# Kernel optimization log

Hardware: AMD Instinct MI355X
Metric: run time of the kernel (lower is better)

The kernel has to match this reference:

```python
import jax, jax.numpy as jnp
import numpy as np
import math

B, H, S, D = 2, 16, 2048, 128
INV_SCALE = math.sqrt(D)  # divisor applied to QK^T logits (dropout_p = 0.0)


def setup_inputs() -> dict:
    key = jax.random.key(0)
    kq, kk, kv = jax.random.split(key, 3)
    return {
        "query": jax.random.normal(kq, (B, H, S, D), dtype=jnp.float32),
        "key": jax.random.normal(kk, (B, H, S, D), dtype=jnp.float32),
        "value": jax.random.normal(kv, (B, H, S, D), dtype=jnp.float32),
    }


def reference(query, key, value):
    # v1 = Q @ K^T ; v2 = v1 / inv_scale ; v3 = softmax(v2, -1) ; dropout(p=0) is identity ; out = v3 @ V
    scores = jnp.einsum("bhqd,bhkd->bhqk", query, key) / INV_SCALE  # [B,H,Sq,Sk]
    probs = jax.nn.softmax(scores, axis=-1)
    return jnp.einsum("bhqk,bhkd->bhqd", probs, value)  # [B,H,Sq,D]
```

## Files before the change

kernel.cpp:

```cpp
#include <hip/hip_runtime.h>
#include <hip/hip_bf16.h>

typedef __bf16 bf16x8 __attribute__((ext_vector_type(8)));
typedef float f32x4 __attribute__((ext_vector_type(4)));

#define S_LEN 2048
#define D_DIM 128
#define BH 32
#define BN 64
#define NT (S_LEN / BN)
#define NWAVE 4
#define QSCALE (0.08838834764831845f * 1.4426950408889634f)


__global__ __launch_bounds__(256, 2)
void fa_fwd_kernel(const float* __restrict__ Qg, const float* __restrict__ Kg,
                   const float* __restrict__ Vg, float* __restrict__ Og) {
    __shared__ __bf16 Klds[BN][D_DIM + 8];
    __shared__ __bf16 Vlds[D_DIM][BN + 8];
    __shared__ __bf16 Plds[NWAVE][32][BN + 8];

    const int bh   = blockIdx.x & (BH - 1);
    const int qt   = blockIdx.x >> 5;
    const int tid  = threadIdx.x;
    const int wave = tid >> 6;
    const int lane = tid & 63;
    const int quad = lane >> 4;
    const int m16  = lane & 15;

    const float* Qh = Qg + bh * (S_LEN * D_DIM);
    const float* Kh = Kg + bh * (S_LEN * D_DIM);
    const float* Vh = Vg + bh * (S_LEN * D_DIM);
    float*       Oh = Og + bh * (S_LEN * D_DIM);

    const int qrow_base = qt * 128 + wave * 32;

    bf16x8 qf[2][4];
#pragma unroll
    for (int mf = 0; mf < 2; ++mf)
#pragma unroll
        for (int ks = 0; ks < 4; ++ks) {
            const float* qp = Qh + (qrow_base + mf * 16 + m16) * D_DIM + ks * 32 + quad * 8;
            const float4 a = *(const float4*)(qp);
            const float4 b = *(const float4*)(qp + 4);
            bf16x8 f;
            f[0] = (__bf16)(a.x * QSCALE); f[1] = (__bf16)(a.y * QSCALE);
            f[2] = (__bf16)(a.z * QSCALE); f[3] = (__bf16)(a.w * QSCALE);
            f[4] = (__bf16)(b.x * QSCALE); f[5] = (__bf16)(b.y * QSCALE);
            f[6] = (__bf16)(b.z * QSCALE); f[7] = (__bf16)(b.w * QSCALE);
            qf[mf][ks] = f;
        }

    f32x4 o_acc[2][8];
#pragma unroll
    for (int mf = 0; mf < 2; ++mf)
#pragma unroll
        for (int nt = 0; nt < 8; ++nt) {
            o_acc[mf][nt][0] = 0.f; o_acc[mf][nt][1] = 0.f;
            o_acc[mf][nt][2] = 0.f; o_acc[mf][nt][3] = 0.f;
        }
    float l_part[2][4] = {{0.f, 0.f, 0.f, 0.f}, {0.f, 0.f, 0.f, 0.f}};

    const int krow = tid >> 4;
    const int kc8  = tid & 15;
    const int vd0   = (tid & 31) * 4;
    const int vgrp  = tid >> 5;
    const int vslot = (vgrp ^ ((vd0 >> 3) & 7)) << 3;

    for (int kt = 0; kt < NT; ++kt) {
        __syncthreads();

        float4 vreg[8];
        {
            const float* vp = Vh + kt * (BN * D_DIM) + vgrp * 8 * D_DIM + vd0;
#pragma unroll
            for (int kr = 0; kr < 8; ++kr)
                vreg[kr] = *(const float4*)(vp + kr * D_DIM);
        }
        float4 kreg[8];
        {
            const float* kg = Kh + kt * (BN * D_DIM);
#pragma unroll
            for (int i = 0; i < 4; ++i) {
                kreg[2 * i]     = *(const float4*)(kg + (krow + 16 * i) * D_DIM + kc8 * 8);
                kreg[2 * i + 1] = *(const float4*)(kg + (krow + 16 * i) * D_DIM + kc8 * 8 + 4);
            }
        }

#pragma unroll
        for (int i = 0; i < 4; ++i) {
            bf16x8 w;
            w[0] = (__bf16)kreg[2 * i].x;     w[1] = (__bf16)kreg[2 * i].y;
            w[2] = (__bf16)kreg[2 * i].z;     w[3] = (__bf16)kreg[2 * i].w;
            w[4] = (__bf16)kreg[2 * i + 1].x; w[5] = (__bf16)kreg[2 * i + 1].y;
            w[6] = (__bf16)kreg[2 * i + 1].z; w[7] = (__bf16)kreg[2 * i + 1].w;
            *(bf16x8*)&Klds[krow + 16 * i][kc8 * 8] = w;
        }

#pragma unroll
        for (int j = 0; j < 4; ++j) {
            bf16x8 w;
#pragma unroll
            for (int kr = 0; kr < 8; ++kr) {
                const float* pv = reinterpret_cast<const float*>(&vreg[kr]);
                w[kr] = (__bf16)pv[j];
            }
            *(bf16x8*)&Vlds[vd0 + j][vslot] = w;
        }
        __syncthreads();

        f32x4 sacc[2][4];
#pragma unroll
        for (int mf = 0; mf < 2; ++mf)
#pragma unroll
            for (int nt = 0; nt < 4; ++nt) {
                sacc[mf][nt][0] = 0.f; sacc[mf][nt][1] = 0.f;
                sacc[mf][nt][2] = 0.f; sacc[mf][nt][3] = 0.f;
            }
        __builtin_amdgcn_s_setprio(1);
#pragma unroll
        for (int ks = 0; ks < 4; ++ks)
#pragma unroll
            for (int nt = 0; nt < 4; ++nt) {
                const bf16x8 kf = *(const bf16x8*)&Klds[nt * 16 + m16][ks * 32 + quad * 8];
                sacc[0][nt] = __builtin_amdgcn_mfma_f32_16x16x32_bf16(qf[0][ks], kf, sacc[0][nt], 0, 0, 0);
                sacc[1][nt] = __builtin_amdgcn_mfma_f32_16x16x32_bf16(qf[1][ks], kf, sacc[1][nt], 0, 0, 0);
            }
        __builtin_amdgcn_s_setprio(0);

#pragma unroll
        for (int mf = 0; mf < 2; ++mf)
#pragma unroll
            for (int nt = 0; nt < 4; ++nt)
#pragma unroll
                for (int r = 0; r < 4; ++r) {
                    const float p = __builtin_amdgcn_exp2f(sacc[mf][nt][r]);
                    l_part[mf][r] += p;
                    Plds[wave][mf * 16 + quad * 4 + r][nt * 16 + m16] = (__bf16)p;
                }

        __builtin_amdgcn_s_setprio(1);
#pragma unroll
        for (int ks = 0; ks < 2; ++ks) {
            const bf16x8 pa0 = *(const bf16x8*)&Plds[wave][m16]     [ks * 32 + quad * 8];
            const bf16x8 pa1 = *(const bf16x8*)&Plds[wave][16 + m16][ks * 32 + quad * 8];
#pragma unroll
            for (int nt = 0; nt < 8; ++nt) {
                const int d = nt * 16 + m16;
                const bf16x8 vf =
                    *(const bf16x8*)&Vlds[d][((ks * 4 + quad) ^ ((d >> 3) & 7)) << 3];
                o_acc[0][nt] = __builtin_amdgcn_mfma_f32_16x16x32_bf16(pa0, vf, o_acc[0][nt], 0, 0, 0);
                o_acc[1][nt] = __builtin_amdgcn_mfma_f32_16x16x32_bf16(pa1, vf, o_acc[1][nt], 0, 0, 0);
            }
        }
        __builtin_amdgcn_s_setprio(0);
    }

#pragma unroll
    for (int xm = 1; xm <= 8; xm <<= 1)
#pragma unroll
        for (int mf = 0; mf < 2; ++mf)
#pragma unroll
            for (int r = 0; r < 4; ++r)
                l_part[mf][r] += __shfl_xor(l_part[mf][r], xm, 64);

#pragma unroll
    for (int mf = 0; mf < 2; ++mf) {
        float inv[4];
#pragma unroll
        for (int r = 0; r < 4; ++r) inv[r] = 1.0f / l_part[mf][r];
#pragma unroll
        for (int nt = 0; nt < 8; ++nt)
#pragma unroll
            for (int r = 0; r < 4; ++r)
                Oh[(qrow_base + mf * 16 + quad * 4 + r) * D_DIM + nt * 16 + m16] =
                    o_acc[mf][nt][r] * inv[r];
    }
}

extern "C" void kernel_launch(void* const* d_in, const int* in_sizes, int n_in,
                              void* d_out, int out_size, void* d_ws, size_t ws_size,
                              hipStream_t stream) {
    const float* Q = (const float*)d_in[0];
    const float* K = (const float*)d_in[1];
    const float* V = (const float*)d_in[2];
    float* O = (float*)d_out;
    dim3 grid(BH * (S_LEN / 128));
    fa_fwd_kernel<<<grid, 256, 0, stream>>>(Q, K, V, O);
}
```

Baseline: 212.3 us.

## Double-buffer K/V tiles, grow Q tile to 256 rows, keep P in registers

Each block now handles 256 query rows (64 per wave), so K/V tiles are reused across twice as many queries. The next K/V tile is prefetched into registers and written to a second LDS buffer while the current one is being computed, leaving one barrier per iteration. QK^T is computed transposed so the exp'd probabilities land in registers already in A-operand layout, which removes the P round-trip through LDS. The grid halves to 256 blocks at one block per CU with much higher register pressure, which risks spills and leaves some CUs idle.

```diff
diff --git a/kernel.cpp b/kernel.cpp
--- a/kernel.cpp
+++ b/kernel.cpp
@@ -2,6 +2,7 @@
 #include <hip/hip_bf16.h>
 
 typedef __bf16 bf16x8 __attribute__((ext_vector_type(8)));
+typedef __bf16 bf16x4 __attribute__((ext_vector_type(4)));
 typedef float f32x4 __attribute__((ext_vector_type(4)));
 
 #define S_LEN 2048
@@ -13,12 +14,11 @@
 #define QSCALE (0.08838834764831845f * 1.4426950408889634f)
 
 
-__global__ __launch_bounds__(256, 2)
+__global__ __launch_bounds__(256, 1)
 void fa_fwd_kernel(const float* __restrict__ Qg, const float* __restrict__ Kg,
                    const float* __restrict__ Vg, float* __restrict__ Og) {
-    __shared__ __bf16 Klds[BN][D_DIM + 8];
-    __shared__ __bf16 Vlds[D_DIM][BN + 8];
-    __shared__ __bf16 Plds[NWAVE][32][BN + 8];
+    __shared__ __bf16 Klds[2][BN][D_DIM + 8];
+    __shared__ __bf16 Vlds[2][D_DIM][BN + 8];
 
     const int bh   = blockIdx.x & (BH - 1);
     const int qt   = blockIdx.x >> 5;
@@ -33,11 +33,11 @@
     const float* Vh = Vg + bh * (S_LEN * D_DIM);
     float*       Oh = Og + bh * (S_LEN * D_DIM);
 
-    const int qrow_base = qt * 128 + wave * 32;
-
-    bf16x8 qf[2][4];
-#pragma unroll
-    for (int mf = 0; mf < 2; ++mf)
+    const int qrow_base = qt * 256 + wave * 64;
+
+    bf16x8 qf[4][4];
+#pragma unroll
+    for (int mf = 0; mf < 4; ++mf)
 #pragma unroll
         for (int ks = 0; ks < 4; ++ks) {
             const float* qp = Qh + (qrow_base + mf * 16 + m16) * D_DIM + ks * 32 + quad * 8;
@@ -51,67 +51,78 @@
             qf[mf][ks] = f;
         }
 
-    f32x4 o_acc[2][8];
-#pragma unroll
-    for (int mf = 0; mf < 2; ++mf)
+    f32x4 o_acc[4][8];
+#pragma unroll
+    for (int mf = 0; mf < 4; ++mf)
 #pragma unroll
         for (int nt = 0; nt < 8; ++nt) {
             o_acc[mf][nt][0] = 0.f; o_acc[mf][nt][1] = 0.f;
             o_acc[mf][nt][2] = 0.f; o_acc[mf][nt][3] = 0.f;
         }
-    float l_part[2][4] = {{0.f, 0.f, 0.f, 0.f}, {0.f, 0.f, 0.f, 0.f}};
-
-    const int krow = tid >> 4;
-    const int kc8  = tid & 15;
-    const int vd0   = (tid & 31) * 4;
-    const int vgrp  = tid >> 5;
-    const int vslot = (vgrp ^ ((vd0 >> 3) & 7)) << 3;
+    float l_part[4] = {0.f, 0.f, 0.f, 0.f};
+
+    const int krow = tid >> 2;
+    const int kc   = (tid & 3) * 32;
+    const int vd0  = lane * 2;
+    const int vgrp = wave;
+    const int vswz  = (vd0 >> 3) & 7;
+    const int rbase = 4 * (vgrp >> 1);
+    const int roff  = 4 * (vgrp & 1);
+
+    float4 kreg[8];
+    float2 vreg[16];
+    {
+        const float* kg = Kh + krow * D_DIM + kc;
+#pragma unroll
+        for (int c = 0; c < 8; ++c)
+            kreg[c] = *(const float4*)(kg + 4 * c);
+        const float* vp = Vh + vgrp * 16 * D_DIM + vd0;
+#pragma unroll
+        for (int kr = 0; kr < 16; ++kr)
+            vreg[kr] = *(const float2*)(vp + kr * D_DIM);
+    }
+    {
+#pragma unroll
+        for (int c = 0; c < 4; ++c) {
+            bf16x8 w;
+            w[0] = (__bf16)kreg[2 * c].x;     w[1] = (__bf16)kreg[2 * c].y;
+            w[2] = (__bf16)kreg[2 * c].z;     w[3] = (__bf16)kreg[2 * c].w;
+            w[4] = (__bf16)kreg[2 * c + 1].x; w[5] = (__bf16)kreg[2 * c + 1].y;
+            w[6] = (__bf16)kreg[2 * c + 1].z; w[7] = (__bf16)kreg[2 * c + 1].w;
+            *(bf16x8*)&Klds[0][krow][kc + 8 * c] = w;
+        }
+#pragma unroll
+        for (int j = 0; j < 4; ++j) {
+            const int colj = (((rbase + j) ^ vswz) << 3) + roff;
+            bf16x4 w0, w1;
+#pragma unroll
+            for (int e = 0; e < 4; ++e) {
+                w0[e] = (__bf16)vreg[4 * j + e].x;
+                w1[e] = (__bf16)vreg[4 * j + e].y;
+            }
+            *(bf16x4*)&Vlds[0][vd0][colj]     = w0;
+            *(bf16x4*)&Vlds[0][vd0 + 1][colj] = w1;
+        }
+    }
+    __syncthreads();
 
     for (int kt = 0; kt < NT; ++kt) {
-        __syncthreads();
-
-        float4 vreg[8];
-        {
-            const float* vp = Vh + kt * (BN * D_DIM) + vgrp * 8 * D_DIM + vd0;
-#pragma unroll
-            for (int kr = 0; kr < 8; ++kr)
-                vreg[kr] = *(const float4*)(vp + kr * D_DIM);
-        }
-        float4 kreg[8];
-        {
-            const float* kg = Kh + kt * (BN * D_DIM);
-#pragma unroll
-            for (int i = 0; i < 4; ++i) {
-                kreg[2 * i]     = *(const float4*)(kg + (krow + 16 * i) * D_DIM + kc8 * 8);
-                kreg[2 * i + 1] = *(const float4*)(kg + (krow + 16 * i) * D_DIM + kc8 * 8 + 4);
-            }
-        }
-
-#pragma unroll
-        for (int i = 0; i < 4; ++i) {
-            bf16x8 w;
-            w[0] = (__bf16)kreg[2 * i].x;     w[1] = (__bf16)kreg[2 * i].y;
-            w[2] = (__bf16)kreg[2 * i].z;     w[3] = (__bf16)kreg[2 * i].w;
-            w[4] = (__bf16)kreg[2 * i + 1].x; w[5] = (__bf16)kreg[2 * i + 1].y;
-            w[6] = (__bf16)kreg[2 * i + 1].z; w[7] = (__bf16)kreg[2 * i + 1].w;
-            *(bf16x8*)&Klds[krow + 16 * i][kc8 * 8] = w;
-        }
-
-#pragma unroll
-        for (int j = 0; j < 4; ++j) {
-            bf16x8 w;
-#pragma unroll
-            for (int kr = 0; kr < 8; ++kr) {
-                const float* pv = reinterpret_cast<const float*>(&vreg[kr]);
-                w[kr] = (__bf16)pv[j];
-            }
-            *(bf16x8*)&Vlds[vd0 + j][vslot] = w;
-        }
-        __syncthreads();
-
-        f32x4 sacc[2][4];
-#pragma unroll
-        for (int mf = 0; mf < 2; ++mf)
+        const int cur = kt & 1;
+
+        if (kt + 1 < NT) {
+            const float* kg = Kh + (kt + 1) * (BN * D_DIM) + krow * D_DIM + kc;
+#pragma unroll
+            for (int c = 0; c < 8; ++c)
+                kreg[c] = *(const float4*)(kg + 4 * c);
+            const float* vp = Vh + (kt + 1) * (BN * D_DIM) + vgrp * 16 * D_DIM + vd0;
+#pragma unroll
+            for (int kr = 0; kr < 16; ++kr)
+                vreg[kr] = *(const float2*)(vp + kr * D_DIM);
+        }
+
+        f32x4 sacc[4][4];
+#pragma unroll
+        for (int mf = 0; mf < 4; ++mf)
 #pragma unroll
             for (int nt = 0; nt < 4; ++nt) {
                 sacc[mf][nt][0] = 0.f; sacc[mf][nt][1] = 0.f;
@@ -122,53 +133,92 @@
         for (int ks = 0; ks < 4; ++ks)
 #pragma unroll
             for (int nt = 0; nt < 4; ++nt) {
-                const bf16x8 kf = *(const bf16x8*)&Klds[nt * 16 + m16][ks * 32 + quad * 8];
-                sacc[0][nt] = __builtin_amdgcn_mfma_f32_16x16x32_bf16(qf[0][ks], kf, sacc[0][nt], 0, 0, 0);
-                sacc[1][nt] = __builtin_amdgcn_mfma_f32_16x16x32_bf16(qf[1][ks], kf, sacc[1][nt], 0, 0, 0);
+                const bf16x8 kf = *(const bf16x8*)&Klds[cur][nt * 16 + m16][ks * 32 + quad * 8];
+                sacc[0][nt] = __builtin_amdgcn_mfma_f32_16x16x32_bf16(kf, qf[0][ks], sacc[0][nt], 0, 0, 0);
+                sacc[1][nt] = __builtin_amdgcn_mfma_f32_16x16x32_bf16(kf, qf[1][ks], sacc[1][nt], 0, 0, 0);
+                sacc[2][nt] = __builtin_amdgcn_mfma_f32_16x16x32_bf16(kf, qf[2][ks], sacc[2][nt], 0, 0, 0);
+                sacc[3][nt] = __builtin_amdgcn_mfma_f32_16x16x32_bf16(kf, qf[3][ks], sacc[3][nt], 0, 0, 0);
             }
         __builtin_amdgcn_s_setprio(0);
 
-#pragma unroll
-        for (int mf = 0; mf < 2; ++mf)
+        bf16x8 pa[4][2];
+#pragma unroll
+        for (int mf = 0; mf < 4; ++mf)
 #pragma unroll
             for (int nt = 0; nt < 4; ++nt)
 #pragma unroll
                 for (int r = 0; r < 4; ++r) {
                     const float p = __builtin_amdgcn_exp2f(sacc[mf][nt][r]);
-                    l_part[mf][r] += p;
-                    Plds[wave][mf * 16 + quad * 4 + r][nt * 16 + m16] = (__bf16)p;
+                    l_part[mf] += p;
+                    pa[mf][nt >> 1][(nt & 1) * 4 + r] = (__bf16)p;
                 }
 
+        bf16x8 vf0[8], vf1[8];
+#pragma unroll
+        for (int nt = 0; nt < 8; ++nt) {
+            const int d = nt * 16 + m16;
+            const int sw = ((d >> 3) & 7) << 3;
+            vf0[nt] = *(const bf16x8*)&Vlds[cur][d][((quad << 3) ^ sw)];
+            vf1[nt] = *(const bf16x8*)&Vlds[cur][d][(((4 + quad) << 3) ^ sw)];
+        }
+
+        if (kt + 1 < NT) {
+            const int nxt = cur ^ 1;
+#pragma unroll
+            for (int c = 0; c < 4; ++c) {
+                bf16x8 w;
+                w[0] = (__bf16)kreg[2 * c].x;     w[1] = (__bf16)kreg[2 * c].y;
+                w[2] = (__bf16)kreg[2 * c].z;     w[3] = (__bf16)kreg[2 * c].w;
+                w[4] = (__bf16)kreg[2 * c + 1].x; w[5] = (__bf16)kreg[2 * c + 1].y;
+                w[6] = (__bf16)kreg[2 * c + 1].z; w[7] = (__bf16)kreg[2 * c + 1].w;
+                *(bf16x8*)&Klds[nxt][krow][kc + 8 * c] = w;
+            }
+#pragma unroll
+            for (int j = 0; j < 4; ++j) {
+                const int colj = (((rbase + j) ^ vswz) << 3) + roff;
+                bf16x4 w0, w1;
+#pragma unroll
+                for (int e = 0; e < 4; ++e) {
+                    w0[e] = (__bf16)vreg[4 * j + e].x;
+                    w1[e] = (__bf16)vreg[4 * j + e].y;
+                }
+                *(bf16x4*)&Vlds[nxt][vd0][colj]     = w0;
+                *(bf16x4*)&Vlds[nxt][vd0 + 1][colj] = w1;
+            }
+        }
+
         __builtin_amdgcn_s_setprio(1);
 #pragma unroll
-        for (int ks = 0; ks < 2; ++ks) {
-            const bf16x8 pa0 = *(const bf16x8*)&Plds[wave][m16]     [ks * 32 + quad * 8];
-            const bf16x8 pa1 = *(const bf16x8*)&Plds[wave][16 + m16][ks * 32 + quad * 8];
-#pragma unroll
-            for (int nt = 0; nt < 8; ++nt) {
-                const int d = nt * 16 + m16;
-                const bf16x8 vf =
-                    *(const bf16x8*)&Vlds[d][((ks * 4 + quad) ^ ((d >> 3) & 7)) << 3];
-                o_acc[0][nt] = __builtin_amdgcn_mfma_f32_16x16x32_bf16(pa0, vf, o_acc[0][nt], 0, 0, 0);
-                o_acc[1][nt] = __builtin_amdgcn_mfma_f32_16x16x32_bf16(pa1, vf, o_acc[1][nt], 0, 0, 0);
-            }
+        for (int nt = 0; nt < 8; ++nt) {
+            o_acc[0][nt] = __builtin_amdgcn_mfma_f32_16x16x32_bf16(pa[0][0], vf0[nt], o_acc[0][nt], 0, 0, 0);
+            o_acc[1][nt] = __builtin_amdgcn_mfma_f32_16x16x32_bf16(pa[1][0], vf0[nt], o_acc[1][nt], 0, 0, 0);
+            o_acc[2][nt] = __builtin_amdgcn_mfma_f32_16x16x32_bf16(pa[2][0], vf0[nt], o_acc[2][nt], 0, 0, 0);
+            o_acc[3][nt] = __builtin_amdgcn_mfma_f32_16x16x32_bf16(pa[3][0], vf0[nt], o_acc[3][nt], 0, 0, 0);
+        }
+#pragma unroll
+        for (int nt = 0; nt < 8; ++nt) {
+            o_acc[0][nt] = __builtin_amdgcn_mfma_f32_16x16x32_bf16(pa[0][1], vf1[nt], o_acc[0][nt], 0, 0, 0);
+            o_acc[1][nt] = __builtin_amdgcn_mfma_f32_16x16x32_bf16(pa[1][1], vf1[nt], o_acc[1][nt], 0, 0, 0);
+            o_acc[2][nt] = __builtin_amdgcn_mfma_f32_16x16x32_bf16(pa[2][1], vf1[nt], o_acc[2][nt], 0, 0, 0);
+            o_acc[3][nt] = __builtin_amdgcn_mfma_f32_16x16x32_bf16(pa[3][1], vf1[nt], o_acc[3][nt], 0, 0, 0);
         }
         __builtin_amdgcn_s_setprio(0);
-    }
-
-#pragma unroll
-    for (int xm = 1; xm <= 8; xm <<= 1)
-#pragma unroll
-        for (int mf = 0; mf < 2; ++mf)
-#pragma unroll
-            for (int r = 0; r < 4; ++r)
-                l_part[mf][r] += __shfl_xor(l_part[mf][r], xm, 64);
-
-#pragma unroll
-    for (int mf = 0; mf < 2; ++mf) {
+
+        __syncthreads();
+    }
+
+#pragma unroll
+    for (int mf = 0; mf < 4; ++mf) {
+        l_part[mf] += __shfl_xor(l_part[mf], 16, 64);
+        l_part[mf] += __shfl_xor(l_part[mf], 32, 64);
+    }
+
+#pragma unroll
+    for (int mf = 0; mf < 4; ++mf) {
+        const float inv_own = 1.0f / l_part[mf];
         float inv[4];
 #pragma unroll
-        for (int r = 0; r < 4; ++r) inv[r] = 1.0f / l_part[mf][r];
+        for (int r = 0; r < 4; ++r) inv[r] = __shfl(inv_own, quad * 4 + r, 64);
 #pragma unroll
         for (int nt = 0; nt < 8; ++nt)
 #pragma unroll
@@ -185,6 +235,6 @@
     const float* K = (const float*)d_in[1];
     const float* V = (const float*)d_in[2];
     float* O = (float*)d_out;
-    dim3 grid(BH * (S_LEN / 128));
+    dim3 grid(BH * (S_LEN / 256));
     fa_fwd_kernel<<<grid, 256, 0, stream>>>(Q, K, V, O);
 }
```

Measured after the change: 241.0 us. +13.5%, slower.
